# Kernel tuning notes

Hardware: AMD Instinct MI355X
Metric: run time of the kernel (lower is better)

Reference implementation:

```python
import jax, jax.numpy as jnp
import numpy as np

B, P, N = 64, 100, 1000
D, H, QD = 128, 8, 16
NUM_GROUPS = 5
MAX_DELTA = 4
SQRT_EMB = float(np.sqrt(D))
CLIP = 10.0
BIAS_INIT = 0.2
BIAS_TAU = 1.0


def setup_inputs() -> dict:
    key = jax.random.key(0)
    ks = jax.random.split(key, 12)
    w_scale = 1.0 / np.sqrt(D)
    encoded_nodes = jax.random.normal(ks[0], (B, N, D), dtype=jnp.float32)
    encoded_q1 = jax.random.normal(ks[1], (B, P, D), dtype=jnp.float32)
    encoded_last_node = jax.random.normal(ks[2], (B, P, D), dtype=jnp.float32)
    ninf_mask = jnp.where(jax.random.uniform(ks[3], (B, P, N)) < 0.2,
                          -jnp.inf, 0.0).astype(jnp.float32)
    Wq_first = (jax.random.normal(ks[4], (D, H * QD)) * w_scale).astype(jnp.float32)
    Wq_last = (jax.random.normal(ks[5], (D, H * QD)) * w_scale).astype(jnp.float32)
    Wk = (jax.random.normal(ks[6], (D, H * QD)) * w_scale).astype(jnp.float32)
    Wv = (jax.random.normal(ks[7], (D, H * QD)) * w_scale).astype(jnp.float32)
    W_comb = (jax.random.normal(ks[8], (H * QD, D)) * w_scale).astype(jnp.float32)
    b_comb = jnp.zeros((D,), dtype=jnp.float32)
    # learnable priority-bias table, init = 0.2 * exp(-delta / tau)
    deltas = jnp.arange(MAX_DELTA + 1, dtype=jnp.float32)
    bias_table = (BIAS_INIT * jnp.exp(-deltas / BIAS_TAU)).astype(jnp.float32)
    group_ids = jax.random.randint(ks[10], (B, N), 0, NUM_GROUPS).astype(jnp.int32)
    current_min_priority = jax.random.randint(ks[11], (B, P), 0, NUM_GROUPS).astype(jnp.int32)
    return {
        'encoded_nodes': encoded_nodes, 'encoded_q1': encoded_q1,
        'encoded_last_node': encoded_last_node, 'ninf_mask': ninf_mask,
        'Wq_first': Wq_first, 'Wq_last': Wq_last, 'Wk': Wk, 'Wv': Wv,
        'W_comb': W_comb, 'b_comb': b_comb, 'bias_table': bias_table,
        'group_ids': group_ids, 'current_min_priority': current_min_priority,
    }


def _heads(x):
    # [B, n, H*QD] -> [B, H, n, QD]
    b, n, _ = x.shape
    return x.reshape(b, n, H, QD).transpose(0, 2, 1, 3)


def reference(encoded_nodes, encoded_q1, encoded_last_node, ninf_mask,
              Wq_first, Wq_last, Wk, Wv, W_comb, b_comb, bias_table,
              group_ids, current_min_priority):
    # set_kv / set_q1
    k = _heads(encoded_nodes @ Wk)            # [B,H,N,QD]
    v = _heads(encoded_nodes @ Wv)            # [B,H,N,QD]
    q_first = _heads(encoded_q1 @ Wq_first)   # [B,H,P,QD]
    # forward
    q_last = _heads(encoded_last_node @ Wq_last)
    q = q_first + q_last
    score = jnp.einsum('bhpd,bhnd->bhpn', q, k) / jnp.sqrt(jnp.float32(QD))
    score = score + ninf_mask[:, None, :, :]  # rank3 ninf mask
    weights = jax.nn.softmax(score, axis=-1)
    out = jnp.einsum('bhpn,bhnd->bhpd', weights, v)
    out_concat = out.transpose(0, 2, 1, 3).reshape(B, P, H * QD)
    mh_atten_out = out_concat @ W_comb + b_comb  # [B,P,D]
    # single-head score against encoder embeddings
    score2 = jnp.einsum('bpd,bnd->bpn', mh_atten_out, encoded_nodes) / SQRT_EMB
    score_clipped = CLIP * jnp.tanh(score2)
    # relative-priority bias gather
    delta = jnp.clip(group_ids[:, None, :] - current_min_priority[:, :, None],
                     0, MAX_DELTA)                     # [B,P,N] int
    priority_bias = bias_table[delta]                  # gather
    priority_bias = jnp.where(jnp.isfinite(ninf_mask), priority_bias, 0.0)
    score_masked = score_clipped + priority_bias + ninf_mask
    probs = jax.nn.softmax(score_masked, axis=-1)
    return probs
```

## Files before the change

kernel.cpp:

```cpp
#include <hip/hip_runtime.h>

#define BB 64
#define PP 100
#define NN 1000
#define DDIM 128
#define HH 8
#define NSPL 8

typedef __attribute__((ext_vector_type(8))) short bf16x8;
typedef __attribute__((ext_vector_type(16))) float f32x16;
typedef __attribute__((ext_vector_type(4))) unsigned u32x4;
typedef __attribute__((ext_vector_type(2))) unsigned u32x2;

__device__ __forceinline__ unsigned bf16rne(float x) {
  unsigned u = __float_as_uint(x);
  return (u + 0x7FFFu + ((u >> 16) & 1u)) >> 16;
}
__device__ __forceinline__ unsigned pk_bf16(float a, float b) {
  return bf16rne(a) | (bf16rne(b) << 16);
}

__device__ __forceinline__ void split8(const float* __restrict__ p,
                                       bf16x8& hi8, bf16x8& lo8) {
  const float4 a = *(const float4*)p;
  const float4 c = *(const float4*)(p + 4);
  float v[8] = {a.x, a.y, a.z, a.w, c.x, c.y, c.z, c.w};
  unsigned hw[4], lw[4];
#pragma unroll
  for (int j = 0; j < 4; ++j) {
    const unsigned h0 = bf16rne(v[2*j]), h1 = bf16rne(v[2*j+1]);
    hw[j] = h0 | (h1 << 16);
    lw[j] = bf16rne(v[2*j]   - __uint_as_float(h0 << 16)) |
            (bf16rne(v[2*j+1] - __uint_as_float(h1 << 16)) << 16);
  }
  hi8 = __builtin_bit_cast(bf16x8, u32x4{hw[0], hw[1], hw[2], hw[3]});
  lo8 = __builtin_bit_cast(bf16x8, u32x4{lw[0], lw[1], lw[2], lw[3]});
}

__global__ __launch_bounds__(256) void pack_w_kernel(
    const float* __restrict__ W0, const float* __restrict__ W1,
    const float* __restrict__ W2, const float* __restrict__ W3,
    const float* __restrict__ W4, u32x4* __restrict__ wfrag)
{
  const int gid = blockIdx.x * 256 + threadIdx.x;
  const int mat = gid >> 11;
  const int ct = (gid >> 9) & 3;
  const int ks = (gid >> 6) & 7;
  const int lane = gid & 63;
  const float* __restrict__ W =
      (mat == 0) ? W0 : (mat == 1) ? W1 : (mat == 2) ? W2 : (mat == 3) ? W3 : W4;
  const int col = ct * 32 + (lane & 31);
  const int k0 = ks * 16 + (lane >> 5) * 8;
  unsigned hi[4], lo[4];
#pragma unroll
  for (int j = 0; j < 4; ++j) {
    const float x0 = W[(k0 + 2 * j) * DDIM + col];
    const float x1 = W[(k0 + 2 * j + 1) * DDIM + col];
    const unsigned h0 = bf16rne(x0), h1 = bf16rne(x1);
    hi[j] = h0 | (h1 << 16);
    lo[j] = bf16rne(x0 - __uint_as_float(h0 << 16)) |
            (bf16rne(x1 - __uint_as_float(h1 << 16)) << 16);
  }
  const int base = (((mat * 4 + ct) * 8 + ks) * 2) * 64 + lane;
  wfrag[base]      = u32x4{hi[0], hi[1], hi[2], hi[3]};
  wfrag[base + 64] = u32x4{lo[0], lo[1], lo[2], lo[3]};
}

__global__ __launch_bounds__(512) void pack_enc_kernel(
    const float* __restrict__ enc, u32x4* __restrict__ encp)
{
  const int b = blockIdx.x >> 5;
  const int t = blockIdx.x & 31;
  const int ks = threadIdx.x >> 6;
  const int lane = threadIdx.x & 63;
  const int n = min(32 * t + (lane & 31), NN - 1);
  const int k0 = ks * 16 + (lane >> 5) * 8;
  bf16x8 hi8, lo8;
  split8(enc + ((size_t)b * NN + n) * DDIM + k0, hi8, lo8);
  const size_t base = ((size_t)(b * 32 + t) * 8 + ks) * 128 + lane;
  encp[base]      = __builtin_bit_cast(u32x4, hi8);
  encp[base + 64] = __builtin_bit_cast(u32x4, lo8);
}

__global__ __launch_bounds__(512) void pack_mh_kernel(
    const float* __restrict__ mh, u32x4* __restrict__ mhp)
{
  const int b = blockIdx.x >> 2;
  const int mt = blockIdx.x & 3;
  const int ks = threadIdx.x >> 6;
  const int lane = threadIdx.x & 63;
  const int p = min(32 * mt + (lane & 31), PP - 1);
  const int k0 = ks * 16 + (lane >> 5) * 8;
  bf16x8 hi8, lo8;
  split8(mh + ((size_t)b * PP + p) * DDIM + k0, hi8, lo8);
  const size_t base = ((size_t)(b * 4 + mt) * 8 + ks) * 128 + lane;
  mhp[base]      = __builtin_bit_cast(u32x4, hi8);
  mhp[base + 64] = __builtin_bit_cast(u32x4, lo8);
}

__global__ __launch_bounds__(256) void proj_kv_mfma_kernel(
    const float* __restrict__ x, const u32x4* __restrict__ wfrag,
    float* __restrict__ outk, float* __restrict__ outv)
{
  const int tid = threadIdx.x;
  const int lane = tid & 63;
  const int wid = tid >> 6;
  const int rtp = wid >> 1;
  const int ctp = wid & 1;
  const int arow = blockIdx.x * 128 + rtp * 64 + (lane & 31);
  const int kgrp = (lane >> 5) * 8;

#pragma unroll 1
  for (int mat = 0; mat < 2; ++mat) {
    float* __restrict__ out = mat ? outv : outk;
    f32x16 acc[2][2];
#pragma unroll
    for (int a = 0; a < 2; ++a)
#pragma unroll
      for (int b = 0; b < 2; ++b)
#pragma unroll
        for (int i = 0; i < 16; ++i) acc[a][b][i] = 0.f;

#pragma unroll 1
    for (int ks = 0; ks < 8; ++ks) {
      bf16x8 ahi[2], alo[2];
#pragma unroll
      for (int rt = 0; rt < 2; ++rt) {
        const float* xp = x + (size_t)(arow + rt * 32) * DDIM + ks * 16 + kgrp;
        split8(xp, ahi[rt], alo[rt]);
      }
#pragma unroll
      for (int ct = 0; ct < 2; ++ct) {
        const int c = ctp * 2 + ct;
        const int fo = (((mat * 4 + c) * 8 + ks) * 2) * 64 + lane;
        const bf16x8 bhi = __builtin_bit_cast(bf16x8, wfrag[fo]);
        const bf16x8 blo = __builtin_bit_cast(bf16x8, wfrag[fo + 64]);
#pragma unroll
        for (int rt = 0; rt < 2; ++rt) {
          acc[rt][ct] = __builtin_amdgcn_mfma_f32_32x32x16_bf16(
              ahi[rt], bhi, acc[rt][ct], 0, 0, 0);
          acc[rt][ct] = __builtin_amdgcn_mfma_f32_32x32x16_bf16(
              ahi[rt], blo, acc[rt][ct], 0, 0, 0);
          acc[rt][ct] = __builtin_amdgcn_mfma_f32_32x32x16_bf16(
              alo[rt], bhi, acc[rt][ct], 0, 0, 0);
        }
      }
    }
#pragma unroll
    for (int rt = 0; rt < 2; ++rt)
#pragma unroll
      for (int ct = 0; ct < 2; ++ct) {
        const int colg = ctp * 64 + ct * 32 + (lane & 31);
        const int rowg0 = blockIdx.x * 128 + rtp * 64 + rt * 32 + 4 * (lane >> 5);
#pragma unroll
        for (int r = 0; r < 16; ++r) {
          const int rowg = rowg0 + (r & 3) + 8 * (r >> 2);
          out[(size_t)rowg * DDIM + colg] = acc[rt][ct][r];
        }
      }
  }
}

__global__ __launch_bounds__(256) void proj_q2_mfma_kernel(
    const float* __restrict__ x1, const float* __restrict__ x2,
    const u32x4* __restrict__ wfrag, float* __restrict__ out, float scale)
{
  const int tid = threadIdx.x;
  const int lane = tid & 63;
  const int w = tid >> 6;
  const int hi = lane >> 5;
  const int l31 = lane & 31;
  const int row0 = blockIdx.x * 128 + w * 32;
  const float* xr1 = x1 + (size_t)(row0 + l31) * DDIM + hi * 8;
  const float* xr2 = x2 + (size_t)(row0 + l31) * DDIM + hi * 8;

  f32x16 acc[4];
#pragma unroll
  for (int ct = 0; ct < 4; ++ct)
#pragma unroll
    for (int i = 0; i < 16; ++i) acc[ct][i] = 0.f;

#pragma unroll 1
  for (int ks = 0; ks < 8; ++ks) {
    bf16x8 a1h, a1l, a2h, a2l;
    split8(xr1 + ks * 16, a1h, a1l);
    split8(xr2 + ks * 16, a2h, a2l);
#pragma unroll
    for (int ct = 0; ct < 4; ++ct) {
      const int fo1 = (((2 * 4 + ct) * 8 + ks) * 2) * 64 + lane;
      const bf16x8 b1h = __builtin_bit_cast(bf16x8, wfrag[fo1]);
      const bf16x8 b1l = __builtin_bit_cast(bf16x8, wfrag[fo1 + 64]);
      acc[ct] = __builtin_amdgcn_mfma_f32_32x32x16_bf16(a1h, b1h, acc[ct], 0, 0, 0);
      acc[ct] = __builtin_amdgcn_mfma_f32_32x32x16_bf16(a1h, b1l, acc[ct], 0, 0, 0);
      acc[ct] = __builtin_amdgcn_mfma_f32_32x32x16_bf16(a1l, b1h, acc[ct], 0, 0, 0);
      const int fo2 = (((3 * 4 + ct) * 8 + ks) * 2) * 64 + lane;
      const bf16x8 b2h = __builtin_bit_cast(bf16x8, wfrag[fo2]);
      const bf16x8 b2l = __builtin_bit_cast(bf16x8, wfrag[fo2 + 64]);
      acc[ct] = __builtin_amdgcn_mfma_f32_32x32x16_bf16(a2h, b2h, acc[ct], 0, 0, 0);
      acc[ct] = __builtin_amdgcn_mfma_f32_32x32x16_bf16(a2h, b2l, acc[ct], 0, 0, 0);
      acc[ct] = __builtin_amdgcn_mfma_f32_32x32x16_bf16(a2l, b2h, acc[ct], 0, 0, 0);
    }
  }
#pragma unroll
  for (int ct = 0; ct < 4; ++ct) {
    const int colg = ct * 32 + l31;
    const int rowg0 = row0 + 4 * hi;
#pragma unroll
    for (int r = 0; r < 16; ++r) {
      const int rowg = rowg0 + (r & 3) + 8 * (r >> 2);
      out[(size_t)rowg * DDIM + colg] = acc[ct][r] * scale;
    }
  }
}

__global__ __launch_bounds__(256) void proj_comb_mfma_kernel(
    const float* __restrict__ x, const u32x4* __restrict__ wfrag,
    const float* __restrict__ bias, float* __restrict__ out)
{
  const int tid = threadIdx.x;
  const int lane = tid & 63;
  const int w = tid >> 6;
  const int hi = lane >> 5;
  const int l31 = lane & 31;
  const int row0 = blockIdx.x * 128 + w * 32;
  const float* xr = x + (size_t)(row0 + l31) * DDIM + hi * 8;

  f32x16 acc[4];
#pragma unroll
  for (int ct = 0; ct < 4; ++ct)
#pragma unroll
    for (int i = 0; i < 16; ++i) acc[ct][i] = 0.f;

#pragma unroll 1
  for (int ks = 0; ks < 8; ++ks) {
    bf16x8 ah, al;
    split8(xr + ks * 16, ah, al);
#pragma unroll
    for (int ct = 0; ct < 4; ++ct) {
      const int fo = (((4 * 4 + ct) * 8 + ks) * 2) * 64 + lane;
      const bf16x8 bh = __builtin_bit_cast(bf16x8, wfrag[fo]);
      const bf16x8 bl = __builtin_bit_cast(bf16x8, wfrag[fo + 64]);
      acc[ct] = __builtin_amdgcn_mfma_f32_32x32x16_bf16(ah, bh, acc[ct], 0, 0, 0);
      acc[ct] = __builtin_amdgcn_mfma_f32_32x32x16_bf16(ah, bl, acc[ct], 0, 0, 0);
      acc[ct] = __builtin_amdgcn_mfma_f32_32x32x16_bf16(al, bh, acc[ct], 0, 0, 0);
    }
  }
#pragma unroll
  for (int ct = 0; ct < 4; ++ct) {
    const int colg = ct * 32 + l31;
    const float bj = bias[colg];
    const int rowg0 = row0 + 4 * hi;
#pragma unroll
    for (int r = 0; r < 16; ++r) {
      const int rowg = rowg0 + (r & 3) + 8 * (r >> 2);
      out[(size_t)rowg * DDIM + colg] = acc[ct][r] + bj;
    }
  }
}

__global__ __launch_bounds__(512) void attn_mfma_kernel(
    const float* __restrict__ Q, const float* __restrict__ K,
    const float* __restrict__ V, const float* __restrict__ mask,
    float* __restrict__ po, float* __restrict__ lsum)
{
  __shared__ float mask_lds[PP * 132];

  const int b = blockIdx.x >> 3;
  const int chunk = blockIdx.x & 7;
  const int n0 = chunk * 128;
  const int tid = threadIdx.x;
  const int h = tid >> 6;
  const int l = tid & 63;
  const int hi = l >> 5;
  const int l31 = l & 31;

  const float NINF = -__builtin_huge_valf();
  for (int idx = tid; idx < PP * 32; idx += 512) {
    const int p = idx >> 5;
    const int c = idx & 31;
    const int nb4 = n0 + 4 * c;
    const int nsrc = min(nb4, NN - 4);
    float4 f = *(const float4*)(mask + ((size_t)(b * PP + p)) * NN + nsrc);
    f.x = (nb4 + 0 < NN) ? f.x : NINF;
    f.y = (nb4 + 1 < NN) ? f.y : NINF;
    f.z = (nb4 + 2 < NN) ? f.z : NINF;
    f.w = (nb4 + 3 < NN) ? f.w : NINF;
    *(float4*)&mask_lds[p * 132 + 4 * c] = f;
  }
  __syncthreads();

  bf16x8 qhi[4], qlo[4];
#pragma unroll
  for (int pt = 0; pt < 4; ++pt) {
    const int qrow = min(b * PP + pt * 32 + l31, BB * PP - 1);
    split8(Q + (size_t)qrow * DDIM + h * 16 + hi * 8, qhi[pt], qlo[pt]);
  }

  f32x16 oacc[4];
#pragma unroll
  for (int pt = 0; pt < 4; ++pt)
#pragma unroll
    for (int i = 0; i < 16; ++i) oacc[pt][i] = 0.f;
  float lacc[4] = {0.f, 0.f, 0.f, 0.f};

  const float* Kb = K + (size_t)b * NN * DDIM + h * 16;
  const float* Vb = V + (size_t)b * NN * DDIM + h * 16;
  const int dv = min(l31, 15);

#pragma unroll 1
  for (int nt = 0; nt < 4; ++nt) {
    const int nb = n0 + nt * 32;

    bf16x8 khi, klo;
    {
      const int krow = min(nb + l31, NN - 1);
      split8(Kb + (size_t)krow * DDIM + hi * 8, khi, klo);
    }
    bf16x8 vhi[2], vlo[2];
#pragma unroll
    for (int ks = 0; ks < 2; ++ks) {
      float vt[8];
#pragma unroll
      for (int i = 0; i < 8; ++i) {
        const int vrow = min(nb + ks * 16 + hi * 8 + i, NN - 1);
        vt[i] = Vb[(size_t)vrow * DDIM + dv];
      }
      unsigned vh[4], vl[4];
#pragma unroll
      for (int j = 0; j < 4; ++j) {
        const unsigned h0 = bf16rne(vt[2*j]), h1 = bf16rne(vt[2*j+1]);
        vh[j] = h0 | (h1 << 16);
        vl[j] = bf16rne(vt[2*j]   - __uint_as_float(h0 << 16)) |
                (bf16rne(vt[2*j+1] - __uint_as_float(h1 << 16)) << 16);
      }
      vhi[ks] = __builtin_bit_cast(bf16x8, u32x4{vh[0], vh[1], vh[2], vh[3]});
      vlo[ks] = __builtin_bit_cast(bf16x8, u32x4{vl[0], vl[1], vl[2], vl[3]});
    }

#pragma unroll
    for (int pt = 0; pt < 4; ++pt) {
      const int prow = min(pt * 32 + l31, PP - 1);
      f32x16 s;
#pragma unroll
      for (int q = 0; q < 4; ++q) {
        const float4 f =
            *(const float4*)&mask_lds[prow * 132 + nt * 32 + q * 8 + hi * 4];
        s[4*q+0] = f.x; s[4*q+1] = f.y; s[4*q+2] = f.z; s[4*q+3] = f.w;
      }
      s = __builtin_amdgcn_mfma_f32_32x32x16_bf16(khi, qhi[pt], s, 0, 0, 0);
      s = __builtin_amdgcn_mfma_f32_32x32x16_bf16(khi, qlo[pt], s, 0, 0, 0);
      s = __builtin_amdgcn_mfma_f32_32x32x16_bf16(klo, qhi[pt], s, 0, 0, 0);

      float ev[16];
#pragma unroll
      for (int r = 0; r < 16; ++r) {
        const float e = __expf(s[r]);
        ev[r] = e;
        lacc[pt] += e;
      }
      unsigned u[8];
#pragma unroll
      for (int j = 0; j < 8; ++j) u[j] = pk_bf16(ev[2*j], ev[2*j+1]);
#pragma unroll
      for (int ks = 0; ks < 2; ++ks) {
        const unsigned t01 = u[ks*4+0], t23 = u[ks*4+1];
        const unsigned t45 = u[ks*4+2], t67 = u[ks*4+3];
        const u32x2 r0 = __builtin_amdgcn_permlane32_swap(t01, t45, false, false);
        const u32x2 r1 = __builtin_amdgcn_permlane32_swap(t23, t67, false, false);
        const bf16x8 pah = __builtin_bit_cast(bf16x8,
            u32x4{r0[0], r1[0], r0[1], r1[1]});
        oacc[pt] = __builtin_amdgcn_mfma_f32_32x32x16_bf16(pah, vhi[ks], oacc[pt], 0, 0, 0);
        oacc[pt] = __builtin_amdgcn_mfma_f32_32x32x16_bf16(pah, vlo[ks], oacc[pt], 0, 0, 0);
      }
    }
  }

  const int base = (b * NSPL + chunk) * PP;
#pragma unroll
  for (int pt = 0; pt < 4; ++pt) {
    const float ltot = lacc[pt] + __shfl_xor(lacc[pt], 32, 64);
    const int pl = pt * 32 + l31;
    if (l < 32 && pl < PP)
      lsum[(size_t)(base + pl) * HH + h] = ltot;
#pragma unroll
    for (int r = 0; r < 16; ++r) {
      const int p = pt * 32 + (r & 3) + 8 * (r >> 2) + 4 * hi;
      if (l31 < 16 && p < PP)
        po[(size_t)(base + p) * DDIM + h * 16 + l31] = oacc[pt][r];
    }
  }
}

__global__ __launch_bounds__(256) void merge_kernel(
    const float* __restrict__ po, const float* __restrict__ lsum,
    float* __restrict__ mh_in)
{
  const int idx = blockIdx.x * 256 + threadIdx.x;
  const int d = idx & 127;
  const int row = idx >> 7;
  const int b = row / PP;
  const int p = row - b * PP;
  const int h = d >> 4;
  float s = 0.f, lt = 0.f;
#pragma unroll
  for (int sp = 0; sp < NSPL; ++sp) {
    const int base = (b * NSPL + sp) * PP + p;
    s  += po[base * DDIM + d];
    lt += lsum[base * HH + h];
  }
  mh_in[idx] = s / lt;
}

__global__ __launch_bounds__(256) void score2_mfma_kernel(
    const u32x4* __restrict__ encp, const u32x4* __restrict__ mhp,
    const float* __restrict__ mask, const float* __restrict__ bias_table,
    const int* __restrict__ group_ids, const int* __restrict__ cur_min,
    float* __restrict__ out, float* __restrict__ ssum)
{
  const int b   = blockIdx.x >> 4;
  const int nc  = blockIdx.x & 15;
  const int n0  = nc * 64;
  const int tid = threadIdx.x;
  const int lane = tid & 63;
  const int mt   = tid >> 6;
  const int half = lane >> 5;
  const int l31  = lane & 31;

  f32x16 acc[2];
#pragma unroll
  for (int c = 0; c < 2; ++c)
#pragma unroll
    for (int i = 0; i < 16; ++i) acc[c][i] = 0.f;

  const u32x4* ma  = mhp  + ((size_t)(b * 4 + mt) * 8) * 128 + lane;
  const u32x4* eb0 = encp + ((size_t)(b * 32 + nc * 2) * 8) * 128 + lane;
  const u32x4* eb1 = encp + ((size_t)(b * 32 + nc * 2 + 1) * 8) * 128 + lane;

#pragma unroll 2
  for (int ks = 0; ks < 8; ++ks) {
    const bf16x8 ahi  = __builtin_bit_cast(bf16x8, ma[ks * 128]);
    const bf16x8 alo  = __builtin_bit_cast(bf16x8, ma[ks * 128 + 64]);
    const bf16x8 bhi0 = __builtin_bit_cast(bf16x8, eb0[ks * 128]);
    const bf16x8 blo0 = __builtin_bit_cast(bf16x8, eb0[ks * 128 + 64]);
    const bf16x8 bhi1 = __builtin_bit_cast(bf16x8, eb1[ks * 128]);
    const bf16x8 blo1 = __builtin_bit_cast(bf16x8, eb1[ks * 128 + 64]);
    acc[0] = __builtin_amdgcn_mfma_f32_32x32x16_bf16(ahi, bhi0, acc[0], 0, 0, 0);
    acc[0] = __builtin_amdgcn_mfma_f32_32x32x16_bf16(ahi, blo0, acc[0], 0, 0, 0);
    acc[0] = __builtin_amdgcn_mfma_f32_32x32x16_bf16(alo, bhi0, acc[0], 0, 0, 0);
    acc[1] = __builtin_amdgcn_mfma_f32_32x32x16_bf16(ahi, bhi1, acc[1], 0, 0, 0);
    acc[1] = __builtin_amdgcn_mfma_f32_32x32x16_bf16(ahi, blo1, acc[1], 0, 0, 0);
    acc[1] = __builtin_amdgcn_mfma_f32_32x32x16_bf16(alo, bhi1, acc[1], 0, 0, 0);
  }

  const float t0 = bias_table[0], t1 = bias_table[1], t2 = bias_table[2],
              t3 = bias_table[3], t4 = bias_table[4];
  const float two_inv_sqrt_emb = 0.1767766952966369f;

  int cmpv[16];
#pragma unroll
  for (int r = 0; r < 16; ++r) {
    const int p = 32 * mt + (r & 3) + 8 * (r >> 2) + 4 * half;
    cmpv[r] = cur_min[b * PP + min(p, PP - 1)];
  }

  float rsum[16];
#pragma unroll
  for (int r = 0; r < 16; ++r) rsum[r] = 0.f;

#pragma unroll
  for (int ct = 0; ct < 2; ++ct) {
    const int n = n0 + ct * 32 + l31;
    const bool nvalid = n < NN;
    const int nr = nvalid ? n : NN - 1;
    const int gid = group_ids[b * NN + nr];
#pragma unroll
    for (int r = 0; r < 16; ++r) {
      const int p = 32 * mt + (r & 3) + 8 * (r >> 2) + 4 * half;
      const bool pvalid = p < PP;
      const int pr = pvalid ? p : PP - 1;
      const float m = mask[((size_t)(b * PP + pr)) * NN + nr];
      const float ex = __expf(acc[ct][r] * two_inv_sqrt_emb);
      const float sc = 10.0f - 20.0f / (ex + 1.0f);
      int delta = gid - cmpv[r];
      delta = delta < 0 ? 0 : (delta > 4 ? 4 : delta);
      const float pb = (delta == 0) ? t0 : (delta == 1) ? t1 : (delta == 2) ? t2
                     : (delta == 3) ? t3 : t4;
      float e = (nvalid && pvalid) ? __expf(sc + pb + m) : 0.0f;
      if (nvalid && pvalid) out[((size_t)(b * PP + p)) * NN + n] = e;
      rsum[r] += e;
    }
  }
#pragma unroll
  for (int r = 0; r < 16; ++r) {
    float ws = rsum[r];
#pragma unroll
    for (int off = 1; off < 32; off <<= 1) ws += __shfl_xor(ws, off, 64);
    rsum[r] = ws;
  }
  if (l31 == 0) {
#pragma unroll
    for (int r = 0; r < 16; ++r) {
      const int p = 32 * mt + (r & 3) + 8 * (r >> 2) + 4 * half;
      if (p < PP) ssum[(size_t)(b * PP + p) * 16 + nc] = rsum[r];
    }
  }
}

__global__ __launch_bounds__(256) void norm_kernel(
    const float* __restrict__ ssum, float* __restrict__ out)
{
  const int row = blockIdx.x;
  float s = 0.f;
#pragma unroll
  for (int i = 0; i < 16; ++i) s += ssum[(size_t)row * 16 + i];
  const float inv = 1.0f / s;
#pragma unroll
  for (int i = 0; i < 4; ++i) {
    const int c = i * 256 + (int)threadIdx.x;
    if (c < NN) out[(size_t)row * NN + c] *= inv;
  }
}

extern "C" void kernel_launch(void* const* d_in, const int* in_sizes, int n_in,
                              void* d_out, int out_size, void* d_ws, size_t ws_size,
                              hipStream_t stream)
{
  (void)in_sizes; (void)n_in; (void)out_size; (void)ws_size;
  const float* enc_nodes  = (const float*)d_in[0];
  const float* enc_q1     = (const float*)d_in[1];
  const float* enc_last   = (const float*)d_in[2];
  const float* ninf       = (const float*)d_in[3];
  const float* Wq_first   = (const float*)d_in[4];
  const float* Wq_last    = (const float*)d_in[5];
  const float* Wk         = (const float*)d_in[6];
  const float* Wv         = (const float*)d_in[7];
  const float* W_comb     = (const float*)d_in[8];
  const float* b_comb     = (const float*)d_in[9];
  const float* bias_table = (const float*)d_in[10];
  const int*   group_ids  = (const int*)d_in[11];
  const int*   cur_min    = (const int*)d_in[12];
  float* out = (float*)d_out;
  float* ws  = (float*)d_ws;

  float* Qw = ws;
  float* Kw = Qw + 819200;
  float* Vw = Kw + 8192000;
  float* po = Vw + 8192000;
  float* ls = po + 6553600;
  float* mh = ls + 409600;
  float* sm = mh + 819200;

  u32x4* wfrag = (u32x4*)sm;
  u32x4* encp = (u32x4*)Kw;
  u32x4* mhp  = ((u32x4*)Kw) + 2097152;

  pack_w_kernel<<<40, 256, 0, stream>>>(Wk, Wv, Wq_first, Wq_last, W_comb, wfrag);
  proj_q2_mfma_kernel<<<BB*PP/128, 256, 0, stream>>>(enc_q1, enc_last, wfrag,
                                                     Qw, 0.25f);
  proj_kv_mfma_kernel<<<BB*NN/128, 256, 0, stream>>>(enc_nodes, wfrag, Kw, Vw);
  attn_mfma_kernel<<<BB*NSPL, 512, 0, stream>>>(Qw, Kw, Vw, ninf, po, ls);
  merge_kernel<<<3200, 256, 0, stream>>>(po, ls, Qw);
  pack_enc_kernel<<<BB*32, 512, 0, stream>>>(enc_nodes, encp);
  proj_comb_mfma_kernel<<<BB*PP/128, 256, 0, stream>>>(Qw, wfrag, b_comb, mh);
  pack_mh_kernel<<<BB*4, 512, 0, stream>>>(mh, mhp);
  score2_mfma_kernel<<<BB*16, 256, 0, stream>>>(encp, mhp, ninf, bias_table,
                                                group_ids, cur_min, out, sm);
  norm_kernel<<<BB*PP, 256, 0, stream>>>(sm, out);
}
```

Before: 176.9 us.

## Emit V from projection in pre-split bf16 MFMA fragment layout

The K/V projection kernel now writes V directly as hi/lo bf16 pairs arranged in the B-operand fragment order the attention kernel consumes, using permlane32 swaps to reorder accumulator rows. The attention kernel replaces its strided scalar V loads and per-iteration bf16 splitting with two vector loads per slice. The projection grid is re-tiled per batch with row clamping, adding some padded work and extra packing math in the projection epilogue.

```diff
diff --git a/kernel.cpp b/kernel.cpp
--- a/kernel.cpp
+++ b/kernel.cpp
@@ -100,34 +100,37 @@
 
 __global__ __launch_bounds__(256) void proj_kv_mfma_kernel(
     const float* __restrict__ x, const u32x4* __restrict__ wfrag,
-    float* __restrict__ outk, float* __restrict__ outv)
+    float* __restrict__ outk, u32x4* __restrict__ vp)
 {
   const int tid = threadIdx.x;
   const int lane = tid & 63;
   const int wid = tid >> 6;
   const int rtp = wid >> 1;
   const int ctp = wid & 1;
-  const int arow = blockIdx.x * 128 + rtp * 64 + (lane & 31);
+  const int b = blockIdx.x >> 3;
+  const int blk8 = blockIdx.x & 7;
+  const int rloc0 = blk8 * 128 + rtp * 64 + (lane & 31);
   const int kgrp = (lane >> 5) * 8;
+  const int l31 = lane & 31;
+  const float* xb = x + (size_t)b * NN * DDIM;
 
 #pragma unroll 1
   for (int mat = 0; mat < 2; ++mat) {
-    float* __restrict__ out = mat ? outv : outk;
     f32x16 acc[2][2];
 #pragma unroll
     for (int a = 0; a < 2; ++a)
 #pragma unroll
-      for (int b = 0; b < 2; ++b)
-#pragma unroll
-        for (int i = 0; i < 16; ++i) acc[a][b][i] = 0.f;
+      for (int c = 0; c < 2; ++c)
+#pragma unroll
+        for (int i = 0; i < 16; ++i) acc[a][c][i] = 0.f;
 
 #pragma unroll 1
     for (int ks = 0; ks < 8; ++ks) {
       bf16x8 ahi[2], alo[2];
 #pragma unroll
       for (int rt = 0; rt < 2; ++rt) {
-        const float* xp = x + (size_t)(arow + rt * 32) * DDIM + ks * 16 + kgrp;
-        split8(xp, ahi[rt], alo[rt]);
+        const int arow = min(rloc0 + rt * 32, NN - 1);
+        split8(xb + (size_t)arow * DDIM + ks * 16 + kgrp, ahi[rt], alo[rt]);
       }
 #pragma unroll
       for (int ct = 0; ct < 2; ++ct) {
@@ -146,18 +149,53 @@
         }
       }
     }
-#pragma unroll
-    for (int rt = 0; rt < 2; ++rt)
-#pragma unroll
-      for (int ct = 0; ct < 2; ++ct) {
-        const int colg = ctp * 64 + ct * 32 + (lane & 31);
-        const int rowg0 = blockIdx.x * 128 + rtp * 64 + rt * 32 + 4 * (lane >> 5);
-#pragma unroll
-        for (int r = 0; r < 16; ++r) {
-          const int rowg = rowg0 + (r & 3) + 8 * (r >> 2);
-          out[(size_t)rowg * DDIM + colg] = acc[rt][ct][r];
+
+    if (mat == 0) {
+#pragma unroll
+      for (int rt = 0; rt < 2; ++rt)
+#pragma unroll
+        for (int ct = 0; ct < 2; ++ct) {
+          const int colg = ctp * 64 + ct * 32 + l31;
+          const int rowl0 = blk8 * 128 + rtp * 64 + rt * 32 + 4 * (lane >> 5);
+#pragma unroll
+          for (int r = 0; r < 16; ++r) {
+            const int rowl = rowl0 + (r & 3) + 8 * (r >> 2);
+            if (rowl < NN)
+              outk[((size_t)b * NN + rowl) * DDIM + colg] = acc[rt][ct][r];
+          }
+        }
+    } else {
+#pragma unroll
+      for (int rt = 0; rt < 2; ++rt) {
+        const int t = blk8 * 4 + rtp * 2 + rt;
+#pragma unroll
+        for (int ct = 0; ct < 2; ++ct) {
+          const int h = ctp * 4 + ct * 2 + (l31 >> 4);
+          const int dcol = l31 & 15;
+#pragma unroll
+          for (int g = 0; g < 2; ++g) {
+            unsigned hw[4], lw[4];
+#pragma unroll
+            for (int j = 0; j < 4; ++j) {
+              const float a0 = acc[rt][ct][8 * g + 2 * j];
+              const float a1 = acc[rt][ct][8 * g + 2 * j + 1];
+              const unsigned h0 = bf16rne(a0), h1 = bf16rne(a1);
+              hw[j] = h0 | (h1 << 16);
+              lw[j] = bf16rne(a0 - __uint_as_float(h0 << 16)) |
+                      (bf16rne(a1 - __uint_as_float(h1 << 16)) << 16);
+            }
+            const u32x2 rh0 = __builtin_amdgcn_permlane32_swap(hw[0], hw[2], false, false);
+            const u32x2 rh1 = __builtin_amdgcn_permlane32_swap(hw[1], hw[3], false, false);
+            const u32x2 rl0 = __builtin_amdgcn_permlane32_swap(lw[0], lw[2], false, false);
+            const u32x2 rl1 = __builtin_amdgcn_permlane32_swap(lw[1], lw[3], false, false);
+            const size_t sb = ((((size_t)(b * 32 + t) * 2 + g) * 8 + h) * 2) * 32
+                              + (lane >> 5) * 16 + dcol;
+            vp[sb]      = u32x4{rh0[0], rh1[0], rh0[1], rh1[1]};
+            vp[sb + 32] = u32x4{rl0[0], rl1[0], rl0[1], rl1[1]};
+          }
         }
       }
+    }
   }
 }
 
@@ -260,7 +298,7 @@
 
 __global__ __launch_bounds__(512) void attn_mfma_kernel(
     const float* __restrict__ Q, const float* __restrict__ K,
-    const float* __restrict__ V, const float* __restrict__ mask,
+    const u32x4* __restrict__ vp, const float* __restrict__ mask,
     float* __restrict__ po, float* __restrict__ lsum)
 {
   __shared__ float mask_lds[PP * 132];
@@ -304,12 +342,11 @@
   float lacc[4] = {0.f, 0.f, 0.f, 0.f};
 
   const float* Kb = K + (size_t)b * NN * DDIM + h * 16;
-  const float* Vb = V + (size_t)b * NN * DDIM + h * 16;
-  const int dv = min(l31, 15);
 
 #pragma unroll 1
   for (int nt = 0; nt < 4; ++nt) {
     const int nb = n0 + nt * 32;
+    const int t = chunk * 4 + nt;
 
     bf16x8 khi, klo;
     {
@@ -319,22 +356,10 @@
     bf16x8 vhi[2], vlo[2];
 #pragma unroll
     for (int ks = 0; ks < 2; ++ks) {
-      float vt[8];
-#pragma unroll
-      for (int i = 0; i < 8; ++i) {
-        const int vrow = min(nb + ks * 16 + hi * 8 + i, NN - 1);
-        vt[i] = Vb[(size_t)vrow * DDIM + dv];
-      }
-      unsigned vh[4], vl[4];
-#pragma unroll
-      for (int j = 0; j < 4; ++j) {
-        const unsigned h0 = bf16rne(vt[2*j]), h1 = bf16rne(vt[2*j+1]);
-        vh[j] = h0 | (h1 << 16);
-        vl[j] = bf16rne(vt[2*j]   - __uint_as_float(h0 << 16)) |
-                (bf16rne(vt[2*j+1] - __uint_as_float(h1 << 16)) << 16);
-      }
-      vhi[ks] = __builtin_bit_cast(bf16x8, u32x4{vh[0], vh[1], vh[2], vh[3]});
-      vlo[ks] = __builtin_bit_cast(bf16x8, u32x4{vl[0], vl[1], vl[2], vl[3]});
+      const size_t sb = ((((size_t)(b * 32 + t) * 2 + ks) * 8 + h) * 2) * 32
+                        + (size_t)hi * 16 + (l31 & 15);
+      vhi[ks] = __builtin_bit_cast(bf16x8, vp[sb]);
+      vlo[ks] = __builtin_bit_cast(bf16x8, vp[sb + 32]);
     }
 
 #pragma unroll
@@ -544,8 +569,8 @@
 
   float* Qw = ws;
   float* Kw = Qw + 819200;
-  float* Vw = Kw + 8192000;
-  float* po = Vw + 8192000;
+  u32x4* Vp = (u32x4*)(Kw + 8192000);
+  float* po = Kw + 8192000 + 8388608;
   float* ls = po + 6553600;
   float* mh = ls + 409600;
   float* sm = mh + 819200;
@@ -557,8 +582,8 @@
   pack_w_kernel<<<40, 256, 0, stream>>>(Wk, Wv, Wq_first, Wq_last, W_comb, wfrag);
   proj_q2_mfma_kernel<<<BB*PP/128, 256, 0, stream>>>(enc_q1, enc_last, wfrag,
                                                      Qw, 0.25f);
-  proj_kv_mfma_kernel<<<BB*NN/128, 256, 0, stream>>>(enc_nodes, wfrag, Kw, Vw);
-  attn_mfma_kernel<<<BB*NSPL, 512, 0, stream>>>(Qw, Kw, Vw, ninf, po, ls);
+  proj_kv_mfma_kernel<<<BB*8, 256, 0, stream>>>(enc_nodes, wfrag, Kw, Vp);
+  attn_mfma_kernel<<<BB*NSPL, 512, 0, stream>>>(Qw, Kw, Vp, ninf, po, ls);
   merge_kernel<<<3200, 256, 0, stream>>>(po, ls, Qw);
   pack_enc_kernel<<<BB*32, 512, 0, stream>>>(enc_nodes, encp);
   proj_comb_mfma_kernel<<<BB*PP/128, 256, 0, stream>>>(Qw, wfrag, b_comb, mh);
```

After: 177.8 us. No clear change (+0.5%).
